# Kernel tuning notes

Hardware: AMD Instinct MI355X
Metric: run time of the kernel (lower is better)

## Reference

```python
import jax, jax.numpy as jnp
import numpy as np

B, T1, D, K = 8, 513, 768, 8192  # batch, tokens incl. CLS, feature dim, codebook size


def setup_inputs() -> dict:
    key = jax.random.key(0)
    k1, k2 = jax.random.split(key)
    representation = jax.random.normal(k1, (B, T1, D), dtype=jnp.float32)
    centroids = jax.random.normal(k2, (K, D), dtype=jnp.float32)
    return {"representation": representation, "centroids": centroids}


def reference(representation, centroids):
    # quant_mem_efficient: drop first (CLS) token, L2-distance argmin over codebook
    rep = representation[:, 1:, :]                        # [B, T, D]
    norm_rep = jnp.sum(rep * rep, axis=-1, keepdims=True)  # [B, T, 1]
    norm_cent = jnp.sum(centroids * centroids, axis=-1)    # [K]
    dot = jnp.einsum('btd,kd->btk', rep, centroids)        # [B, T, K]
    distances = norm_rep + norm_cent[None, None, :] - 2.0 * dot
    tokens = jnp.argmin(distances, axis=-1)                # [B, T] int
    # unquant: embedding gather
    quantized = jnp.take(centroids, tokens, axis=0)        # [B, T, D]
    return tokens, quantized
```

## Files before the change

### kernel.cpp

```cpp
#include <hip/hip_runtime.h>
#include <stdint.h>

#define BT 4096
#define KC 8192
#define DD 768
#define T_STRIDE 513
#define DELTA 6.0f

typedef _Float16 f16x8 __attribute__((ext_vector_type(8)));
typedef _Float16 f16x4 __attribute__((ext_vector_type(4)));
typedef float    f32x4 __attribute__((ext_vector_type(4)));

#define GLD16(gp, lp)                                                       \
  __builtin_amdgcn_global_load_lds(                                         \
      (__attribute__((address_space(1))) void*)(gp),                        \
      (__attribute__((address_space(3))) void*)(lp), 16, 0, 0)

__device__ __forceinline__ unsigned int sortable_bits(float d) {
  unsigned int bits = __float_as_uint(d);
  return (bits & 0x80000000u) ? ~bits : (bits | 0x80000000u);
}

__global__ __launch_bounds__(256) void split_norm_kernel(
    const float* __restrict__ rep, const float* __restrict__ cent,
    _Float16* __restrict__ a_hi, _Float16* __restrict__ b_hi,
    float* __restrict__ norm_rep, float* __restrict__ norm_cent) {
  int wid  = (blockIdx.x * blockDim.x + threadIdx.x) >> 6;
  int lane = threadIdx.x & 63;
  const float* src;
  _Float16* hi;
  float* nd;
  if (wid < BT) {
    int b = wid >> 9, tt = wid & 511;
    src = rep + (size_t)(b * T_STRIDE + 1 + tt) * DD;
    hi = a_hi ? a_hi + (size_t)wid * DD : nullptr;
    nd = norm_rep + wid;
  } else {
    int k = wid - BT;
    if (k >= KC) return;
    src = cent + (size_t)k * DD;
    hi = b_hi ? b_hi + (size_t)k * DD : nullptr;
    nd = norm_cent + k;
  }
  const float4* s4 = (const float4*)src;
  f16x4* h4 = (f16x4*)hi;
  float s = 0.f;
  #pragma unroll
  for (int i = 0; i < 3; ++i) {
    float4 v = s4[lane + i * 64];
    s += v.x * v.x + v.y * v.y + v.z * v.z + v.w * v.w;
    if (hi) {
      f16x4 h;
      h[0] = (_Float16)v.x; h[1] = (_Float16)v.y;
      h[2] = (_Float16)v.z; h[3] = (_Float16)v.w;
      h4[lane + i * 64] = h;
    }
  }
  #pragma unroll
  for (int off = 32; off; off >>= 1) s += __shfl_down(s, off, 64);
  if (lane == 0) *nd = s;
}

__global__ __launch_bounds__(256, 2) void mfma_dist_cand(
    const _Float16* __restrict__ a_hi,
    const _Float16* __restrict__ b_hi,
    const float* __restrict__ norm_rep, const float* __restrict__ norm_cent,
    float* __restrict__ LMin, unsigned long long* __restrict__ Mask) {
  __shared__ _Float16 As[128 * 64];
  __shared__ _Float16 Bs[128 * 64];

  const int tid = threadIdx.x;
  const int w = tid >> 6, l = tid & 63;
  const int bm0 = blockIdx.x * 128;
  const int bn0 = blockIdx.y * 128;

  const int srow   = l >> 3;
  const int schunk = (l & 7) ^ srow;
  size_t goffA[4], goffB[4];
  _Float16 *ldsA[4], *ldsB[4];
  #pragma unroll
  for (int j2 = 0; j2 < 4; ++j2) {
    const int j = w * 4 + j2;
    goffA[j2] = (size_t)(bm0 + j * 8 + srow) * DD + schunk * 8;
    goffB[j2] = (size_t)(bn0 + j * 8 + srow) * DD + schunk * 8;
    ldsA[j2] = As + j * 8 * 64;
    ldsB[j2] = Bs + j * 8 * 64;
  }

  const int wm = (w & 1) * 64;
  const int wn = (w >> 1) * 64;
  const int sub = l & 15, q = l >> 4;

  f32x4 acc[4][4] = {};

  for (int kin = 0; kin < DD; kin += 64) {
    __syncthreads();
    #pragma unroll
    for (int j2 = 0; j2 < 4; ++j2) {
      GLD16(b_hi + goffA[j2] + kin, ldsA[j2]);
      GLD16(a_hi + goffB[j2] + kin, ldsB[j2]);
    }
    __syncthreads();

    #pragma unroll
    for (int kk = 0; kk < 2; ++kk) {
      f16x8 af[4], bfr[4];
      #pragma unroll
      for (int i = 0; i < 4; ++i) {
        const int arow = wm + i * 16 + sub;
        const int brow = wn + i * 16 + sub;
        const int c = q + kk * 4;
        af[i]  = *(const f16x8*)(As + arow * 64 + ((c ^ (arow & 7)) * 8));
        bfr[i] = *(const f16x8*)(Bs + brow * 64 + ((c ^ (brow & 7)) * 8));
      }
      #pragma unroll
      for (int mt = 0; mt < 4; ++mt)
        #pragma unroll
        for (int nt = 0; nt < 4; ++nt)
          acc[mt][nt] = __builtin_amdgcn_mfma_f32_16x16x32_f16(
              af[mt], bfr[nt], acc[mt][nt], 0, 0, 0);
    }
  }

  const int g = blockIdx.x * 2 + (w & 1);
  float ncv[4][4];
  #pragma unroll
  for (int mt = 0; mt < 4; ++mt)
    #pragma unroll
    for (int r = 0; r < 4; ++r)
      ncv[mt][r] = norm_cent[bm0 + wm + mt * 16 + q * 4 + r];

  #pragma unroll
  for (int nt = 0; nt < 4; ++nt) {
    const int t = bn0 + wn + nt * 16 + sub;
    const float nr = norm_rep[t];
    float d[4][4];
    float dmin = 3.4e38f;
    #pragma unroll
    for (int mt = 0; mt < 4; ++mt)
      #pragma unroll
      for (int r = 0; r < 4; ++r) {
        d[mt][r] = (nr + ncv[mt][r]) - 2.0f * acc[mt][nt][r];
        dmin = fminf(dmin, d[mt][r]);
      }
    dmin = fminf(dmin, __shfl_xor(dmin, 16, 64));
    dmin = fminf(dmin, __shfl_xor(dmin, 32, 64));
    const float thresh = dmin + DELTA;
    unsigned long long pm = 0;
    #pragma unroll
    for (int mt = 0; mt < 4; ++mt)
      #pragma unroll
      for (int r = 0; r < 4; ++r)
        if (d[mt][r] <= thresh) pm |= 1ull << (mt * 16 + q * 4 + r);
    pm |= (unsigned long long)__shfl_xor((long long)pm, 16, 64);
    pm |= (unsigned long long)__shfl_xor((long long)pm, 32, 64);
    if (q == 0) {
      LMin[(size_t)t * 128 + g] = dmin;
      Mask[(size_t)t * 128 + g] = pm;
    }
  }
}

__global__ __launch_bounds__(256) void refine_kernel(
    const float* __restrict__ LMin, const unsigned long long* __restrict__ Mask,
    const float* __restrict__ rep, const float* __restrict__ cent,
    const float* __restrict__ norm_rep, const float* __restrict__ norm_cent,
    float* __restrict__ out_tokens, float* __restrict__ out_q) {
  __shared__ float s_min[4];
  __shared__ int s_half[128];
  __shared__ int s_cnt;
  __shared__ unsigned long long s_bestw[4];
  __shared__ int s_kbest;

  const int t = blockIdx.x;
  const int tid = threadIdx.x;
  const int w = tid >> 6, l = tid & 63;

  if (tid == 0) s_cnt = 0;
  float lm = (tid < 128) ? LMin[(size_t)t * 128 + tid] : 3.4e38f;
  float v = lm;
  #pragma unroll
  for (int off = 32; off; off >>= 1) v = fminf(v, __shfl_xor(v, off, 64));
  if (l == 0) s_min[w] = v;
  __syncthreads();
  const float gmin = fminf(fminf(s_min[0], s_min[1]), fminf(s_min[2], s_min[3]));
  const float thresh = gmin + DELTA;
  if (tid < 128 && lm <= thresh) {
    int idx = atomicAdd(&s_cnt, 1);
    s_half[idx] = tid;
  }
  __syncthreads();
  const int cnt = s_cnt;

  const int b_ = t >> 9, tt = t & 511;
  const float* rrow = rep + (size_t)(b_ * T_STRIDE + 1 + tt) * DD;
  const float nr = norm_rep[t];
  unsigned long long bestE = ~0ull;
  int cno = 0;

  for (int c = 0; c < cnt; ++c) {
    const int h = s_half[c];
    unsigned long long mask = Mask[(size_t)t * 128 + h];
    while (mask) {
      const int bit = __ffsll((unsigned long long)mask) - 1;
      mask &= mask - 1;
      if ((cno++ & 3) == w) {
        const int k = h * 64 + bit;
        const float* crow = cent + (size_t)k * DD;
        float part = 0.f;
        #pragma unroll
        for (int j = 0; j < 12; ++j)
          part += rrow[l + j * 64] * crow[l + j * 64];
        #pragma unroll
        for (int off = 32; off; off >>= 1) part += __shfl_down(part, off, 64);
        if (l == 0) {
          float d = (nr + norm_cent[k]) - 2.0f * part;
          unsigned long long p =
              ((unsigned long long)sortable_bits(d) << 32) | (unsigned)k;
          if (p < bestE) bestE = p;
        }
      }
    }
  }
  if (l == 0) s_bestw[w] = bestE;
  __syncthreads();
  if (tid == 0) {
    unsigned long long b = s_bestw[0];
    #pragma unroll
    for (int i = 1; i < 4; ++i) if (s_bestw[i] < b) b = s_bestw[i];
    s_kbest = (int)(b & 0xFFFFFFFFull);
    out_tokens[t] = (float)s_kbest;
  }
  __syncthreads();
  const int kbest = s_kbest;
  if (tid < 192) {
    const float4* src = (const float4*)(cent + (size_t)kbest * DD);
    float4* dst = (float4*)(out_q + (size_t)t * DD);
    dst[tid] = src[tid];
  }
}

#define FBM 64
#define FBN 64
#define FBK 16
#define FNSPLIT 16
__global__ __launch_bounds__(256) void fp32_argmin_gemm(
    const float* __restrict__ rep, const float* __restrict__ cent,
    const float* __restrict__ norm_rep, const float* __restrict__ norm_cent,
    unsigned long long* __restrict__ packed) {
  __shared__ float Asf[FBK][FBM];
  __shared__ float Bsf[FBK][FBN];
  const int tid = threadIdx.x;
  const int m0  = blockIdx.x * FBM;
  const int kbase = blockIdx.y * (KC / FNSPLIT);
  const int tx = tid & 15, ty = tid >> 4;
  const int ldr = tid >> 2, ldc = (tid & 3) * 4;
  const int t_ld = m0 + ldr;
  const float* arow =
      rep + (size_t)((t_ld >> 9) * T_STRIDE + 1 + (t_ld & 511)) * DD + ldc;
  unsigned long long best[4];
  #pragma unroll
  for (int i = 0; i < 4; ++i) best[i] = ~0ull;
  float nr[4];
  #pragma unroll
  for (int i = 0; i < 4; ++i) nr[i] = norm_rep[m0 + ty * 4 + i];
  for (int nt = 0; nt < (KC / FNSPLIT) / FBN; ++nt) {
    const int n0 = kbase + nt * FBN;
    const float* brow = cent + (size_t)(n0 + ldr) * DD + ldc;
    float acc[4][4];
    #pragma unroll
    for (int i = 0; i < 4; ++i)
      #pragma unroll
      for (int j = 0; j < 4; ++j) acc[i][j] = 0.f;
    for (int d0 = 0; d0 < DD; d0 += FBK) {
      float4 av = *(const float4*)(arow + d0);
      float4 bv = *(const float4*)(brow + d0);
      __syncthreads();
      Asf[ldc + 0][ldr] = av.x; Asf[ldc + 1][ldr] = av.y;
      Asf[ldc + 2][ldr] = av.z; Asf[ldc + 3][ldr] = av.w;
      Bsf[ldc + 0][ldr] = bv.x; Bsf[ldc + 1][ldr] = bv.y;
      Bsf[ldc + 2][ldr] = bv.z; Bsf[ldc + 3][ldr] = bv.w;
      __syncthreads();
      #pragma unroll
      for (int kk = 0; kk < FBK; ++kk) {
        float4 a4 = *(const float4*)&Asf[kk][ty * 4];
        float4 b4 = *(const float4*)&Bsf[kk][tx * 4];
        float a[4] = {a4.x, a4.y, a4.z, a4.w};
        float b[4] = {b4.x, b4.y, b4.z, b4.w};
        #pragma unroll
        for (int i = 0; i < 4; ++i)
          #pragma unroll
          for (int j = 0; j < 4; ++j) acc[i][j] += a[i] * b[j];
      }
    }
    #pragma unroll
    for (int i = 0; i < 4; ++i) {
      #pragma unroll
      for (int j = 0; j < 4; ++j) {
        int k = n0 + tx * 4 + j;
        float d = (nr[i] + norm_cent[k]) - 2.0f * acc[i][j];
        unsigned long long p =
            ((unsigned long long)sortable_bits(d) << 32) | (unsigned int)k;
        if (p < best[i]) best[i] = p;
      }
    }
  }
  #pragma unroll
  for (int off = 1; off < 16; off <<= 1) {
    #pragma unroll
    for (int i = 0; i < 4; ++i) {
      unsigned long long o =
          (unsigned long long)__shfl_xor((long long)best[i], off, 64);
      if (o < best[i]) best[i] = o;
    }
  }
  if (tx == 0) {
    #pragma unroll
    for (int i = 0; i < 4; ++i)
      atomicMin(&packed[m0 + ty * 4 + i], best[i]);
  }
}

__global__ __launch_bounds__(192) void gather_kernel(
    const unsigned long long* __restrict__ packed,
    const float* __restrict__ cent,
    float* __restrict__ out_tokens, float* __restrict__ out_q) {
  int t = blockIdx.x;
  unsigned int k = (unsigned int)(packed[t] & 0xFFFFFFFFull);
  if (threadIdx.x == 0) out_tokens[t] = (float)k;
  const float4* src = (const float4*)(cent + (size_t)k * DD);
  float4* dst = (float4*)(out_q + (size_t)t * DD);
  dst[threadIdx.x] = src[threadIdx.x];
}

extern "C" void kernel_launch(void* const* d_in, const int* in_sizes, int n_in,
                              void* d_out, int out_size, void* d_ws, size_t ws_size,
                              hipStream_t stream) {
  const float* rep  = (const float*)d_in[0];
  const float* cent = (const float*)d_in[1];
  float* out = (float*)d_out;

  const size_t SZ_AH = (size_t)BT * DD * 2;
  const size_t SZ_BH = (size_t)KC * DD * 2;
  const size_t SZ_LM = (size_t)BT * 128 * 4;
  const size_t SZ_MK = (size_t)BT * 128 * 8;
  const size_t WS_A  = SZ_AH + SZ_BH + SZ_LM + SZ_MK + 49152;

  if (ws_size >= WS_A) {
    _Float16* a_hi = (_Float16*)d_ws;
    _Float16* b_hi = (_Float16*)((char*)d_ws + SZ_AH);
    float* LMin    = (float*)((char*)d_ws + SZ_AH + SZ_BH);
    unsigned long long* Mask =
        (unsigned long long*)((char*)d_ws + SZ_AH + SZ_BH + SZ_LM);
    float* norm_rep  = (float*)((char*)d_ws + SZ_AH + SZ_BH + SZ_LM + SZ_MK);
    float* norm_cent = (float*)((char*)d_ws + SZ_AH + SZ_BH + SZ_LM + SZ_MK + 16384);

    split_norm_kernel<<<3072, 256, 0, stream>>>(rep, cent, a_hi, b_hi,
                                                norm_rep, norm_cent);
    dim3 grid(KC / 128, BT / 128);
    mfma_dist_cand<<<grid, 256, 0, stream>>>(a_hi, b_hi, norm_rep, norm_cent,
                                             LMin, Mask);
    refine_kernel<<<BT, 256, 0, stream>>>(LMin, Mask, rep, cent, norm_rep,
                                          norm_cent, out, out + BT);
  } else {
    unsigned long long* packed = (unsigned long long*)d_ws;
    float* norm_rep  = (float*)((char*)d_ws + 32768);
    float* norm_cent = (float*)((char*)d_ws + 49152);

    hipMemsetAsync(packed, 0xFF, BT * sizeof(unsigned long long), stream);
    split_norm_kernel<<<3072, 256, 0, stream>>>(rep, cent, nullptr, nullptr,
                                                norm_rep, norm_cent);
    dim3 grid(BT / FBM, FNSPLIT);
    fp32_argmin_gemm<<<grid, 256, 0, stream>>>(rep, cent, norm_rep, norm_cent,
                                               packed);
    gather_kernel<<<BT, 192, 0, stream>>>(packed, cent, out, out + BT);
  }
}
```

Measured before the change: 146.1 us.

## Fuse candidate refinement into GEMM via last-block-done counter, drop row norms

Merges the fp16 MFMA candidate kernel and the fp32 refine kernel into one launch. Each group of 64 blocks sharing a token tile bumps an atomic counter, and the last block to finish refines those 128 tokens, one wave per token. The per-token norm_rep term is dropped because it does not change the argmin, which removes its computation and loads. The risk is that refinement now runs on only 32 blocks, serialised with one wave per token, so it could become a tail that costs more than the launch it removes.

```diff
diff --git a/kernel.cpp b/kernel.cpp
--- a/kernel.cpp
+++ b/kernel.cpp
@@ -24,55 +24,59 @@
 __global__ __launch_bounds__(256) void split_norm_kernel(
     const float* __restrict__ rep, const float* __restrict__ cent,
     _Float16* __restrict__ a_hi, _Float16* __restrict__ b_hi,
-    float* __restrict__ norm_rep, float* __restrict__ norm_cent) {
+    float* __restrict__ norm_cent) {
   int wid  = (blockIdx.x * blockDim.x + threadIdx.x) >> 6;
   int lane = threadIdx.x & 63;
-  const float* src;
-  _Float16* hi;
-  float* nd;
   if (wid < BT) {
     int b = wid >> 9, tt = wid & 511;
-    src = rep + (size_t)(b * T_STRIDE + 1 + tt) * DD;
-    hi = a_hi ? a_hi + (size_t)wid * DD : nullptr;
-    nd = norm_rep + wid;
-  } else {
-    int k = wid - BT;
-    if (k >= KC) return;
-    src = cent + (size_t)k * DD;
-    hi = b_hi ? b_hi + (size_t)k * DD : nullptr;
-    nd = norm_cent + k;
-  }
-  const float4* s4 = (const float4*)src;
-  f16x4* h4 = (f16x4*)hi;
-  float s = 0.f;
-  #pragma unroll
-  for (int i = 0; i < 3; ++i) {
-    float4 v = s4[lane + i * 64];
-    s += v.x * v.x + v.y * v.y + v.z * v.z + v.w * v.w;
-    if (hi) {
+    const float4* s4 = (const float4*)(rep + (size_t)(b * T_STRIDE + 1 + tt) * DD);
+    f16x4* h4 = (f16x4*)(a_hi + (size_t)wid * DD);
+    #pragma unroll
+    for (int i = 0; i < 3; ++i) {
+      float4 v = s4[lane + i * 64];
       f16x4 h;
       h[0] = (_Float16)v.x; h[1] = (_Float16)v.y;
       h[2] = (_Float16)v.z; h[3] = (_Float16)v.w;
       h4[lane + i * 64] = h;
     }
-  }
-  #pragma unroll
-  for (int off = 32; off; off >>= 1) s += __shfl_down(s, off, 64);
-  if (lane == 0) *nd = s;
-}
-
-__global__ __launch_bounds__(256, 2) void mfma_dist_cand(
-    const _Float16* __restrict__ a_hi,
-    const _Float16* __restrict__ b_hi,
-    const float* __restrict__ norm_rep, const float* __restrict__ norm_cent,
-    float* __restrict__ LMin, unsigned long long* __restrict__ Mask) {
+  } else {
+    int k = wid - BT;
+    if (k >= KC) return;
+    const float4* s4 = (const float4*)(cent + (size_t)k * DD);
+    f16x4* h4 = (f16x4*)(b_hi + (size_t)k * DD);
+    float s = 0.f;
+    #pragma unroll
+    for (int i = 0; i < 3; ++i) {
+      float4 v = s4[lane + i * 64];
+      s += v.x * v.x + v.y * v.y + v.z * v.z + v.w * v.w;
+      f16x4 h;
+      h[0] = (_Float16)v.x; h[1] = (_Float16)v.y;
+      h[2] = (_Float16)v.z; h[3] = (_Float16)v.w;
+      h4[lane + i * 64] = h;
+    }
+    #pragma unroll
+    for (int off = 32; off; off >>= 1) s += __shfl_down(s, off, 64);
+    if (lane == 0) norm_cent[k] = s;
+  }
+}
+
+__global__ __launch_bounds__(256, 2) void gemm_refine(
+    const _Float16* __restrict__ a_hi, const _Float16* __restrict__ b_hi,
+    const float* __restrict__ rep, const float* __restrict__ cent,
+    const float* __restrict__ norm_cent,
+    unsigned* __restrict__ LMin,
+    unsigned long long* __restrict__ Mask,
+    unsigned* __restrict__ cnt,
+    float* __restrict__ out_tokens, float* __restrict__ out_q) {
   __shared__ _Float16 As[128 * 64];
   __shared__ _Float16 Bs[128 * 64];
+  __shared__ unsigned s_old;
 
   const int tid = threadIdx.x;
   const int w = tid >> 6, l = tid & 63;
-  const int bm0 = blockIdx.x * 128;
-  const int bn0 = blockIdx.y * 128;
+  const int bn  = blockIdx.x >> 6;
+  const int bm0 = (blockIdx.x & 63) * 128;
+  const int bn0 = bn * 128;
 
   const int srow   = l >> 3;
   const int schunk = (l & 7) ^ srow;
@@ -122,7 +126,7 @@
     }
   }
 
-  const int g = blockIdx.x * 2 + (w & 1);
+  const int g = (bm0 >> 6) + (w & 1);
   float ncv[4][4];
   #pragma unroll
   for (int mt = 0; mt < 4; ++mt)
@@ -133,14 +137,13 @@
   #pragma unroll
   for (int nt = 0; nt < 4; ++nt) {
     const int t = bn0 + wn + nt * 16 + sub;
-    const float nr = norm_rep[t];
     float d[4][4];
     float dmin = 3.4e38f;
     #pragma unroll
     for (int mt = 0; mt < 4; ++mt)
       #pragma unroll
       for (int r = 0; r < 4; ++r) {
-        d[mt][r] = (nr + ncv[mt][r]) - 2.0f * acc[mt][nt][r];
+        d[mt][r] = ncv[mt][r] - 2.0f * acc[mt][nt][r];
         dmin = fminf(dmin, d[mt][r]);
       }
     dmin = fminf(dmin, __shfl_xor(dmin, 16, 64));
@@ -155,88 +158,75 @@
     pm |= (unsigned long long)__shfl_xor((long long)pm, 16, 64);
     pm |= (unsigned long long)__shfl_xor((long long)pm, 32, 64);
     if (q == 0) {
-      LMin[(size_t)t * 128 + g] = dmin;
-      Mask[(size_t)t * 128 + g] = pm;
-    }
-  }
-}
-
-__global__ __launch_bounds__(256) void refine_kernel(
-    const float* __restrict__ LMin, const unsigned long long* __restrict__ Mask,
-    const float* __restrict__ rep, const float* __restrict__ cent,
-    const float* __restrict__ norm_rep, const float* __restrict__ norm_cent,
-    float* __restrict__ out_tokens, float* __restrict__ out_q) {
-  __shared__ float s_min[4];
-  __shared__ int s_half[128];
-  __shared__ int s_cnt;
-  __shared__ unsigned long long s_bestw[4];
-  __shared__ int s_kbest;
-
-  const int t = blockIdx.x;
-  const int tid = threadIdx.x;
-  const int w = tid >> 6, l = tid & 63;
-
-  if (tid == 0) s_cnt = 0;
-  float lm = (tid < 128) ? LMin[(size_t)t * 128 + tid] : 3.4e38f;
-  float v = lm;
-  #pragma unroll
-  for (int off = 32; off; off >>= 1) v = fminf(v, __shfl_xor(v, off, 64));
-  if (l == 0) s_min[w] = v;
+      __hip_atomic_store(&LMin[(size_t)t * 128 + g], __float_as_uint(dmin),
+                         __ATOMIC_RELAXED, __HIP_MEMORY_SCOPE_AGENT);
+      __hip_atomic_store(&Mask[(size_t)t * 128 + g], pm,
+                         __ATOMIC_RELAXED, __HIP_MEMORY_SCOPE_AGENT);
+    }
+  }
+
+  __threadfence();
   __syncthreads();
-  const float gmin = fminf(fminf(s_min[0], s_min[1]), fminf(s_min[2], s_min[3]));
-  const float thresh = gmin + DELTA;
-  if (tid < 128 && lm <= thresh) {
-    int idx = atomicAdd(&s_cnt, 1);
-    s_half[idx] = tid;
-  }
+  if (tid == 0)
+    s_old = __hip_atomic_fetch_add(&cnt[bn], 1u, __ATOMIC_ACQ_REL,
+                                   __HIP_MEMORY_SCOPE_AGENT);
   __syncthreads();
-  const int cnt = s_cnt;
-
-  const int b_ = t >> 9, tt = t & 511;
-  const float* rrow = rep + (size_t)(b_ * T_STRIDE + 1 + tt) * DD;
-  const float nr = norm_rep[t];
-  unsigned long long bestE = ~0ull;
-  int cno = 0;
-
-  for (int c = 0; c < cnt; ++c) {
-    const int h = s_half[c];
-    unsigned long long mask = Mask[(size_t)t * 128 + h];
-    while (mask) {
-      const int bit = __ffsll((unsigned long long)mask) - 1;
-      mask &= mask - 1;
-      if ((cno++ & 3) == w) {
-        const int k = h * 64 + bit;
-        const float* crow = cent + (size_t)k * DD;
-        float part = 0.f;
-        #pragma unroll
-        for (int j = 0; j < 12; ++j)
-          part += rrow[l + j * 64] * crow[l + j * 64];
-        #pragma unroll
-        for (int off = 32; off; off >>= 1) part += __shfl_down(part, off, 64);
-        if (l == 0) {
-          float d = (nr + norm_cent[k]) - 2.0f * part;
-          unsigned long long p =
-              ((unsigned long long)sortable_bits(d) << 32) | (unsigned)k;
-          if (p < bestE) bestE = p;
+  if (s_old != 63) return;
+  __threadfence();
+
+  for (int i = 0; i < 32; ++i) {
+    const int t = bn0 + w * 32 + i;
+    const float lm0 = __uint_as_float(__hip_atomic_load(
+        &LMin[(size_t)t * 128 + l], __ATOMIC_RELAXED, __HIP_MEMORY_SCOPE_AGENT));
+    const float lm1 = __uint_as_float(__hip_atomic_load(
+        &LMin[(size_t)t * 128 + 64 + l], __ATOMIC_RELAXED, __HIP_MEMORY_SCOPE_AGENT));
+    float v = fminf(lm0, lm1);
+    #pragma unroll
+    for (int off = 32; off; off >>= 1) v = fminf(v, __shfl_xor(v, off, 64));
+    const float thresh = v + DELTA;
+    unsigned long long gm0 = __ballot(lm0 <= thresh);
+    unsigned long long gm1 = __ballot(lm1 <= thresh);
+
+    const int b_ = t >> 9, tt = t & 511;
+    const float* rrow = rep + (size_t)(b_ * T_STRIDE + 1 + tt) * DD;
+    unsigned long long bestE = ~0ull;
+
+    #pragma unroll
+    for (int half = 0; half < 2; ++half) {
+      unsigned long long gmask = half ? gm1 : gm0;
+      while (gmask) {
+        const int h = __ffsll((unsigned long long)gmask) - 1;
+        gmask &= gmask - 1;
+        unsigned long long mask = __hip_atomic_load(
+            &Mask[(size_t)t * 128 + half * 64 + h], __ATOMIC_RELAXED,
+            __HIP_MEMORY_SCOPE_AGENT);
+        while (mask) {
+          const int bit = __ffsll((unsigned long long)mask) - 1;
+          mask &= mask - 1;
+          const int k = (half * 64 + h) * 64 + bit;
+          const float* crow = cent + (size_t)k * DD;
+          float part = 0.f;
+          #pragma unroll
+          for (int j = 0; j < 12; ++j)
+            part += rrow[l + j * 64] * crow[l + j * 64];
+          #pragma unroll
+          for (int off = 32; off; off >>= 1) part += __shfl_down(part, off, 64);
+          if (l == 0) {
+            float d = norm_cent[k] - 2.0f * part;
+            unsigned long long p =
+                ((unsigned long long)sortable_bits(d) << 32) | (unsigned)k;
+            if (p < bestE) bestE = p;
+          }
         }
       }
     }
-  }
-  if (l == 0) s_bestw[w] = bestE;
-  __syncthreads();
-  if (tid == 0) {
-    unsigned long long b = s_bestw[0];
-    #pragma unroll
-    for (int i = 1; i < 4; ++i) if (s_bestw[i] < b) b = s_bestw[i];
-    s_kbest = (int)(b & 0xFFFFFFFFull);
-    out_tokens[t] = (float)s_kbest;
-  }
-  __syncthreads();
-  const int kbest = s_kbest;
-  if (tid < 192) {
+    int kb0 = (l == 0) ? (int)(bestE & 0xFFFFFFFFull) : 0;
+    const int kbest = __shfl(kb0, 0, 64);
+    if (l == 0) out_tokens[t] = (float)kbest;
     const float4* src = (const float4*)(cent + (size_t)kbest * DD);
     float4* dst = (float4*)(out_q + (size_t)t * DD);
-    dst[tid] = src[tid];
+    #pragma unroll
+    for (int j = 0; j < 3; ++j) dst[l + j * 64] = src[l + j * 64];
   }
 }
 
@@ -244,6 +234,30 @@
 #define FBN 64
 #define FBK 16
 #define FNSPLIT 16
+__global__ __launch_bounds__(256) void norms_only_kernel(
+    const float* __restrict__ rep, const float* __restrict__ cent,
+    float* __restrict__ norm_rep, float* __restrict__ norm_cent) {
+  int wid  = (blockIdx.x * blockDim.x + threadIdx.x) >> 6;
+  int lane = threadIdx.x & 63;
+  const float* src;
+  float* nd;
+  if (wid < BT) {
+    int b = wid >> 9, tt = wid & 511;
+    src = rep + (size_t)(b * T_STRIDE + 1 + tt) * DD;
+    nd = norm_rep + wid;
+  } else {
+    int k = wid - BT;
+    if (k >= KC) return;
+    src = cent + (size_t)k * DD;
+    nd = norm_cent + k;
+  }
+  float s = 0.f;
+  for (int j = lane; j < DD; j += 64) { float v = src[j]; s += v * v; }
+  #pragma unroll
+  for (int off = 32; off; off >>= 1) s += __shfl_down(s, off, 64);
+  if (lane == 0) *nd = s;
+}
+
 __global__ __launch_bounds__(256) void fp32_argmin_gemm(
     const float* __restrict__ rep, const float* __restrict__ cent,
     const float* __restrict__ norm_rep, const float* __restrict__ norm_cent,
@@ -344,32 +358,31 @@
   const size_t SZ_BH = (size_t)KC * DD * 2;
   const size_t SZ_LM = (size_t)BT * 128 * 4;
   const size_t SZ_MK = (size_t)BT * 128 * 8;
-  const size_t WS_A  = SZ_AH + SZ_BH + SZ_LM + SZ_MK + 49152;
+  const size_t OFF_NC  = SZ_AH + SZ_BH + SZ_LM + SZ_MK;
+  const size_t OFF_CNT = OFF_NC + 32768;
+  const size_t WS_A    = OFF_CNT + 256;
 
   if (ws_size >= WS_A) {
     _Float16* a_hi = (_Float16*)d_ws;
     _Float16* b_hi = (_Float16*)((char*)d_ws + SZ_AH);
-    float* LMin    = (float*)((char*)d_ws + SZ_AH + SZ_BH);
+    unsigned* LMin = (unsigned*)((char*)d_ws + SZ_AH + SZ_BH);
     unsigned long long* Mask =
         (unsigned long long*)((char*)d_ws + SZ_AH + SZ_BH + SZ_LM);
-    float* norm_rep  = (float*)((char*)d_ws + SZ_AH + SZ_BH + SZ_LM + SZ_MK);
-    float* norm_cent = (float*)((char*)d_ws + SZ_AH + SZ_BH + SZ_LM + SZ_MK + 16384);
-
+    float* norm_cent = (float*)((char*)d_ws + OFF_NC);
+    unsigned* cnt    = (unsigned*)((char*)d_ws + OFF_CNT);
+
+    hipMemsetAsync(cnt, 0, 32 * sizeof(unsigned), stream);
     split_norm_kernel<<<3072, 256, 0, stream>>>(rep, cent, a_hi, b_hi,
-                                                norm_rep, norm_cent);
-    dim3 grid(KC / 128, BT / 128);
-    mfma_dist_cand<<<grid, 256, 0, stream>>>(a_hi, b_hi, norm_rep, norm_cent,
-                                             LMin, Mask);
-    refine_kernel<<<BT, 256, 0, stream>>>(LMin, Mask, rep, cent, norm_rep,
-                                          norm_cent, out, out + BT);
+                                                norm_cent);
+    gemm_refine<<<2048, 256, 0, stream>>>(a_hi, b_hi, rep, cent, norm_cent,
+                                          LMin, Mask, cnt, out, out + BT);
   } else {
     unsigned long long* packed = (unsigned long long*)d_ws;
     float* norm_rep  = (float*)((char*)d_ws + 32768);
     float* norm_cent = (float*)((char*)d_ws + 49152);
 
     hipMemsetAsync(packed, 0xFF, BT * sizeof(unsigned long long), stream);
-    split_norm_kernel<<<3072, 256, 0, stream>>>(rep, cent, nullptr, nullptr,
-                                                norm_rep, norm_cent);
+    norms_only_kernel<<<3072, 256, 0, stream>>>(rep, cent, norm_rep, norm_cent);
     dim3 grid(BT / FBM, FNSPLIT);
     fp32_argmin_gemm<<<grid, 256, 0, stream>>>(rep, cent, norm_rep, norm_cent,
                                                packed);
```

New measurement: 498.4 us. 241% more time.
